# Optimization experiments

Measured on AMD Instinct MI355X. Metric: run time of the kernel, lower is better.

Reference implementation:

```python
import jax, jax.numpy as jnp
import numpy as np

PSIZE = 3
PSTRIDE = 3
N = PSIZE * PSTRIDE   # 9 attention tokens
P = PSIZE ** 2        # 9 pixels per token


def setup_inputs() -> dict:
    key = jax.random.key(0)
    k1, k2, k3, k4, k5 = jax.random.split(key, 5)
    B, H, W, C = 8192, 9, 9, 256
    hidden = C // 2
    x = jax.random.normal(k1, (B, H, W, C), dtype=jnp.float32)
    W_fc = jax.random.normal(k2, (hidden, C), dtype=jnp.float32) * (C ** -0.5)
    b_fc = jax.random.normal(k3, (hidden,), dtype=jnp.float32) * 0.01
    block_idx = jax.random.randint(k4, (B,), 0, 1024, dtype=jnp.int32)
    match_vec = jax.random.randint(k5, (1024, 1), 0, 2, dtype=jnp.int32)
    return {"x": x, "W_fc": W_fc, "b_fc": b_fc, "block_idx": block_idx, "match_vec": match_vec}


def reference(x, W_fc, b_fc, block_idx, match_vec):
    B, H, Wd, C = x.shape
    hidden = W_fc.shape[0]
    scale = (hidden * P) ** -0.5

    # [B, pstride, psize, pstride, psize, C] -> patch-major [B, ps, ps, p, p, C]
    xv = x.reshape(B, PSTRIDE, PSIZE, PSTRIDE, PSIZE, C).transpose(0, 1, 3, 2, 4, 5)
    x_fc = xv.reshape(B, N, P, C)

    # linear projection C -> hidden, then flatten pixels: q [B, N, P*hidden]
    q = (jnp.einsum('bnpc,hc->bnph', x_fc, W_fc) + b_fc).reshape(B, N, P * hidden)

    attn = jnp.einsum('bnd,bmd->bnm', q, q) * scale  # [B, N, N]

    # additive mask: -100 on diagonal, zeroed out entirely for matched samples
    base = jnp.where(jnp.eye(N, dtype=bool), jnp.float32(-100.0), jnp.float32(0.0))
    cur_match = match_vec[block_idx].squeeze(-1)  # [B]
    mask = jnp.where(cur_match[:, None, None] == 1, jnp.float32(0.0), base[None])

    attn = jax.nn.softmax(attn + mask, axis=-1)

    v = xv.reshape(B, N, P * C)
    out = attn @ v  # [B, N, P*C]

    out = out.reshape(B, PSTRIDE, PSTRIDE, PSIZE, PSIZE, C)
    out = out.transpose(0, 1, 3, 2, 4, 5).reshape(B, H, Wd, C)
    return out
```

## Files before the change

### kernel.cpp

```cpp
#include <hip/hip_runtime.h>

typedef short short8 __attribute__((ext_vector_type(8)));
typedef float floatx16 __attribute__((ext_vector_type(16)));
typedef float floatx4 __attribute__((ext_vector_type(4)));
typedef unsigned int uint4v __attribute__((ext_vector_type(4)));

#define ROWS 81
#define CDIM 256
#define QOFF 41472
#define SOFF 62208
#define ABOFF 63232
#define SMEM_TOTAL 63744

__device__ __forceinline__ unsigned short f2bf(float f) {
    union { float f; unsigned int u; } v; v.f = f;
    return (unsigned short)((v.u + 0x7FFFu + ((v.u >> 16) & 1u)) >> 16);
}

__global__ void wconv_kernel(const float* __restrict__ W,
                             unsigned short* __restrict__ Wb, int n) {
    int i = blockIdx.x * 256 + threadIdx.x;
    if (i < n) Wb[i] = f2bf(W[i]);
}

__global__ __launch_bounds__(512, 4)
void attn_kernel(const float* __restrict__ x,
                 const unsigned short* __restrict__ Wb,
                 const float* __restrict__ b_fc,
                 const int* __restrict__ block_idx,
                 const int* __restrict__ match_vec,
                 float* __restrict__ out)
{
    __shared__ __align__(16) char smem[SMEM_TOTAL];
    const int b     = blockIdx.x;
    const int t     = threadIdx.x;
    const int lane  = t & 63;
    const int wave  = t >> 6;
    const int l15   = lane & 15;
    const int kg    = lane >> 4;
    const int l31   = lane & 31;
    const int khalf = lane >> 5;

    int cur_match = 0;
    if (t < 9) cur_match = match_vec[block_idx[b]];

    short8 wfrag[8];
    {
        const unsigned short* wr = Wb + (wave * 16 + l15) * CDIM + kg * 8;
#pragma unroll
        for (int ks = 0; ks < 8; ++ks)
            wfrag[ks] = *(const short8*)(wr + ks * 32);
    }
    const float bias = b_fc[wave * 16 + l15];

    {
        const float* xb = x + (long)b * (ROWS * CDIM);
        for (int k = t; k < ROWS * 32; k += 512) {
            int gr = k >> 5;
            int c0 = (k & 31) * 8;
            float4 a0 = *(const float4*)(xb + gr * CDIM + c0);
            float4 a1 = *(const float4*)(xb + gr * CDIM + c0 + 4);
            int hh = gr / 9, ww = gr % 9;
            int r = ((hh / 3) * 3 + (ww / 3)) * 9 + ((hh % 3) * 3 + (ww % 3));
            short8 v;
            v[0] = (short)f2bf(a0.x); v[1] = (short)f2bf(a0.y);
            v[2] = (short)f2bf(a0.z); v[3] = (short)f2bf(a0.w);
            v[4] = (short)f2bf(a1.x); v[5] = (short)f2bf(a1.y);
            v[6] = (short)f2bf(a1.z); v[7] = (short)f2bf(a1.w);
            int off = r * 512 + ((c0 * 2) ^ ((r & 15) << 4));
            *(short8*)(smem + off) = v;
        }
    }
    __syncthreads();

    floatx4 acc[6];
#pragma unroll
    for (int i = 0; i < 6; ++i)
#pragma unroll
        for (int j = 0; j < 4; ++j) acc[i][j] = 0.f;
    const int swl = l15 << 4;
#pragma unroll
    for (int ks = 0; ks < 8; ++ks) {
        int cb = ks * 64 + kg * 16;
#pragma unroll
        for (int tile = 0; tile < 6; ++tile) {
            int r = tile * 16 + l15;
            short8 a = *(const short8*)(smem + r * 512 + (cb ^ swl));
            acc[tile] = __builtin_amdgcn_mfma_f32_16x16x32_bf16(a, wfrag[ks], acc[tile], 0, 0, 0);
        }
    }

    {
        int h2 = (wave * 16 + l15) * 2;
#pragma unroll
        for (int tile = 0; tile < 6; ++tile) {
#pragma unroll
            for (int reg = 0; reg < 4; ++reg) {
                int r = tile * 16 + kg * 4 + reg;
                if (r < ROWS)
                    *(unsigned short*)(smem + QOFF + r * 256 + (h2 ^ ((r & 15) << 4))) =
                        f2bf(acc[tile][reg] + bias);
            }
        }
    }
    __syncthreads();

    if (wave == 0) {
        floatx4 s0, s1, s2, s3;
#pragma unroll
        for (int i = 0; i < 4; ++i) { s0[i] = 0.f; s1[i] = 0.f; s2[i] = 0.f; s3[i] = 0.f; }
        int nc = (l15 < 9) ? l15 : 8;
#pragma unroll
        for (int s = 0; s < 9; ++s) {
#pragma unroll
            for (int i = 0; i < 4; ++i) {
                int ks = i * 9 + s;
                int k  = ks * 32 + kg * 8;
                int p  = k >> 7;
                int h0 = (k & 127) * 2;
                int row = nc * 9 + p;
                short8 f = *(const short8*)(smem + QOFF + row * 256 + (h0 ^ ((row & 15) << 4)));
                floatx4 tmp = __builtin_amdgcn_mfma_f32_16x16x32_bf16(f, f, (i==0?s0:i==1?s1:i==2?s2:s3), 0, 0, 0);
                if (i == 0) s0 = tmp; else if (i == 1) s1 = tmp; else if (i == 2) s2 = tmp; else s3 = tmp;
            }
        }
        float* sc = (float*)(smem + SOFF);
#pragma unroll
        for (int reg = 0; reg < 4; ++reg)
            sc[(kg * 4 + reg) * 16 + l15] = s0[reg] + s1[reg] + s2[reg] + s3[reg];
    }
    __syncthreads();

    if (t < 9) {
        const float scale = 0.029462782549439483f;
        float* sc = (float*)(smem + SOFF);
        float s[9];
        float mx = -1e30f;
#pragma unroll
        for (int m = 0; m < 9; ++m) {
            float v = sc[t * 16 + m] * scale;
            if (m == t && cur_match != 1) v -= 100.f;
            s[m] = v;
            mx = fmaxf(mx, v);
        }
        float sum = 0.f;
#pragma unroll
        for (int m = 0; m < 9; ++m) { s[m] = __expf(s[m] - mx); sum += s[m]; }
        float inv = 1.f / sum;
        unsigned short* ab = (unsigned short*)(smem + ABOFF) + t * 16;
#pragma unroll
        for (int m = 0; m < 9; ++m) ab[m] = f2bf(s[m] * inv);
#pragma unroll
        for (int m = 9; m < 16; ++m) ab[m] = 0;
    }
    __syncthreads();

    {
        const int n  = l31;
        const int nm = (n < 9) ? n : 0;
        short8 bf = *(const short8*)(smem + ABOFF + nm * 32 + khalf * 16);
        float* ob = out + (long)b * (ROWS * CDIM);
        int hh = 0, ww = 0;
        if (n < 9) { hh = (n / 3) * 3; ww = (n % 3) * 3; }
#pragma unroll
        for (int tt = 0; tt < 9; ++tt) {
            int tile = wave * 9 + tt;
            int d = tile * 32 + l31;
            int p = d >> 8, c = d & 255;
            short8 af;
#pragma unroll
            for (int j = 0; j < 8; ++j) {
                int m = khalf * 8 + j; if (m > 8) m = 8;
                int row = m * 9 + p;
                af[j] = *(const short*)(smem + row * 512 + ((c * 2) ^ ((row & 15) << 4)));
            }
            floatx16 dacc;
#pragma unroll
            for (int i = 0; i < 16; ++i) dacc[i] = 0.f;
            dacc = __builtin_amdgcn_mfma_f32_32x32x16_bf16(af, bf, dacc, 0, 0, 0);
            if (n < 9) {
#pragma unroll
                for (int q2 = 0; q2 < 4; ++q2) {
                    int d0 = tile * 32 + q2 * 8 + khalf * 4;
                    int p0 = d0 >> 8, c0 = d0 & 255;
                    int gr = (hh + (p0 / 3)) * 9 + (ww + (p0 % 3));
                    *(float4*)(ob + gr * CDIM + c0) =
                        make_float4(dacc[q2 * 4 + 0], dacc[q2 * 4 + 1],
                                    dacc[q2 * 4 + 2], dacc[q2 * 4 + 3]);
                }
            }
        }
    }
}

extern "C" void kernel_launch(void* const* d_in, const int* in_sizes, int n_in,
                              void* d_out, int out_size, void* d_ws, size_t ws_size,
                              hipStream_t stream) {
    const float* x    = (const float*)d_in[0];
    const float* W    = (const float*)d_in[1];
    const float* bfc  = (const float*)d_in[2];
    const int*   bidx = (const int*)d_in[3];
    const int*   mvec = (const int*)d_in[4];
    float* outp = (float*)d_out;
    unsigned short* Wb = (unsigned short*)d_ws;

    int nW = in_sizes[1];
    wconv_kernel<<<(nW + 255) / 256, 256, 0, stream>>>(W, Wb, nW);

    int B = in_sizes[0] / (ROWS * CDIM);
    attn_kernel<<<B, 512, 0, stream>>>(x, Wb, bfc, bidx, mvec, outp);
}
```

Before: 371.4 us.

## Make attention kernel persistent with register prefetch of next sample

Launches a fixed grid of 512 blocks, each looping over a contiguous range of batch samples. W fragments and bias are loaded once per block. The next sample's input is prefetched into registers in two halves while the current sample's projection and score phases run, then written to shared memory after the output phase. This hides global load latency and amortizes per-block setup. The cost is higher register pressure, an extra barrier per iteration, and only 512 blocks, which may leave CUs underfilled relative to 4 blocks per CU.

```diff
diff --git a/kernel.cpp b/kernel.cpp
--- a/kernel.cpp
+++ b/kernel.cpp
@@ -3,7 +3,6 @@
 typedef short short8 __attribute__((ext_vector_type(8)));
 typedef float floatx16 __attribute__((ext_vector_type(16)));
 typedef float floatx4 __attribute__((ext_vector_type(4)));
-typedef unsigned int uint4v __attribute__((ext_vector_type(4)));
 
 #define ROWS 81
 #define CDIM 256
@@ -23,16 +22,29 @@
     if (i < n) Wb[i] = f2bf(W[i]);
 }
 
+__device__ __forceinline__ void stage_store(char* smem, int k, float4 a0, float4 a1) {
+    int gr = k >> 5;
+    int c0 = (k & 31) * 8;
+    int hh = gr / 9, ww = gr - hh * 9;
+    int r = ((hh / 3) * 3 + (ww / 3)) * 9 + ((hh % 3) * 3 + (ww % 3));
+    short8 v;
+    v[0] = (short)f2bf(a0.x); v[1] = (short)f2bf(a0.y);
+    v[2] = (short)f2bf(a0.z); v[3] = (short)f2bf(a0.w);
+    v[4] = (short)f2bf(a1.x); v[5] = (short)f2bf(a1.y);
+    v[6] = (short)f2bf(a1.z); v[7] = (short)f2bf(a1.w);
+    *(short8*)(smem + r * 512 + ((c0 * 2) ^ ((r & 15) << 4))) = v;
+}
+
 __global__ __launch_bounds__(512, 4)
 void attn_kernel(const float* __restrict__ x,
                  const unsigned short* __restrict__ Wb,
                  const float* __restrict__ b_fc,
                  const int* __restrict__ block_idx,
                  const int* __restrict__ match_vec,
-                 float* __restrict__ out)
+                 float* __restrict__ out,
+                 int B, int nIter)
 {
     __shared__ __align__(16) char smem[SMEM_TOTAL];
-    const int b     = blockIdx.x;
     const int t     = threadIdx.x;
     const int lane  = t & 63;
     const int wave  = t >> 6;
@@ -40,9 +52,8 @@
     const int kg    = lane >> 4;
     const int l31   = lane & 31;
     const int khalf = lane >> 5;
-
-    int cur_match = 0;
-    if (t < 9) cur_match = match_vec[block_idx[b]];
+    const int base  = blockIdx.x * nIter;
+    if (base >= B) return;
 
     short8 wfrag[8];
     {
@@ -52,144 +63,193 @@
             wfrag[ks] = *(const short8*)(wr + ks * 32);
     }
     const float bias = b_fc[wave * 16 + l15];
+    const int swl = l15 << 4;
 
     {
-        const float* xb = x + (long)b * (ROWS * CDIM);
-        for (int k = t; k < ROWS * 32; k += 512) {
-            int gr = k >> 5;
-            int c0 = (k & 31) * 8;
-            float4 a0 = *(const float4*)(xb + gr * CDIM + c0);
-            float4 a1 = *(const float4*)(xb + gr * CDIM + c0 + 4);
-            int hh = gr / 9, ww = gr % 9;
-            int r = ((hh / 3) * 3 + (ww / 3)) * 9 + ((hh % 3) * 3 + (ww % 3));
-            short8 v;
-            v[0] = (short)f2bf(a0.x); v[1] = (short)f2bf(a0.y);
-            v[2] = (short)f2bf(a0.z); v[3] = (short)f2bf(a0.w);
-            v[4] = (short)f2bf(a1.x); v[5] = (short)f2bf(a1.y);
-            v[6] = (short)f2bf(a1.z); v[7] = (short)f2bf(a1.w);
-            int off = r * 512 + ((c0 * 2) ^ ((r & 15) << 4));
-            *(short8*)(smem + off) = v;
-        }
+        const float* xb = x + (size_t)base * (ROWS * CDIM);
+        float4 a0[3], a1[3];
+#pragma unroll
+        for (int j = 0; j < 3; ++j) {
+            int k = t + 512 * j;
+            a0[j] = *(const float4*)(xb + k * 8);
+            a1[j] = *(const float4*)(xb + k * 8 + 4);
+        }
+#pragma unroll
+        for (int j = 0; j < 3; ++j) stage_store(smem, t + 512 * j, a0[j], a1[j]);
+#pragma unroll
+        for (int j = 0; j < 2; ++j) {
+            int k = t + 1536 + 512 * j;
+            a0[j] = *(const float4*)(xb + k * 8);
+            a1[j] = *(const float4*)(xb + k * 8 + 4);
+        }
+        if (t < 32) {
+            a0[2] = *(const float4*)(xb + (t + 2560) * 8);
+            a1[2] = *(const float4*)(xb + (t + 2560) * 8 + 4);
+        }
+#pragma unroll
+        for (int j = 0; j < 2; ++j) stage_store(smem, t + 1536 + 512 * j, a0[j], a1[j]);
+        if (t < 32) stage_store(smem, t + 2560, a0[2], a1[2]);
     }
     __syncthreads();
 
-    floatx4 acc[6];
-#pragma unroll
-    for (int i = 0; i < 6; ++i)
-#pragma unroll
-        for (int j = 0; j < 4; ++j) acc[i][j] = 0.f;
-    const int swl = l15 << 4;
-#pragma unroll
-    for (int ks = 0; ks < 8; ++ks) {
-        int cb = ks * 64 + kg * 16;
-#pragma unroll
-        for (int tile = 0; tile < 6; ++tile) {
-            int r = tile * 16 + l15;
-            short8 a = *(const short8*)(smem + r * 512 + (cb ^ swl));
-            acc[tile] = __builtin_amdgcn_mfma_f32_16x16x32_bf16(a, wfrag[ks], acc[tile], 0, 0, 0);
-        }
-    }
-
-    {
-        int h2 = (wave * 16 + l15) * 2;
-#pragma unroll
-        for (int tile = 0; tile < 6; ++tile) {
-#pragma unroll
-            for (int reg = 0; reg < 4; ++reg) {
-                int r = tile * 16 + kg * 4 + reg;
-                if (r < ROWS)
-                    *(unsigned short*)(smem + QOFF + r * 256 + (h2 ^ ((r & 15) << 4))) =
-                        f2bf(acc[tile][reg] + bias);
-            }
-        }
-    }
-    __syncthreads();
-
-    if (wave == 0) {
-        floatx4 s0, s1, s2, s3;
-#pragma unroll
-        for (int i = 0; i < 4; ++i) { s0[i] = 0.f; s1[i] = 0.f; s2[i] = 0.f; s3[i] = 0.f; }
-        int nc = (l15 < 9) ? l15 : 8;
-#pragma unroll
-        for (int s = 0; s < 9; ++s) {
-#pragma unroll
-            for (int i = 0; i < 4; ++i) {
-                int ks = i * 9 + s;
-                int k  = ks * 32 + kg * 8;
-                int p  = k >> 7;
-                int h0 = (k & 127) * 2;
-                int row = nc * 9 + p;
-                short8 f = *(const short8*)(smem + QOFF + row * 256 + (h0 ^ ((row & 15) << 4)));
-                floatx4 tmp = __builtin_amdgcn_mfma_f32_16x16x32_bf16(f, f, (i==0?s0:i==1?s1:i==2?s2:s3), 0, 0, 0);
-                if (i == 0) s0 = tmp; else if (i == 1) s1 = tmp; else if (i == 2) s2 = tmp; else s3 = tmp;
-            }
-        }
-        float* sc = (float*)(smem + SOFF);
-#pragma unroll
-        for (int reg = 0; reg < 4; ++reg)
-            sc[(kg * 4 + reg) * 16 + l15] = s0[reg] + s1[reg] + s2[reg] + s3[reg];
-    }
-    __syncthreads();
-
-    if (t < 9) {
-        const float scale = 0.029462782549439483f;
-        float* sc = (float*)(smem + SOFF);
-        float s[9];
-        float mx = -1e30f;
-#pragma unroll
-        for (int m = 0; m < 9; ++m) {
-            float v = sc[t * 16 + m] * scale;
-            if (m == t && cur_match != 1) v -= 100.f;
-            s[m] = v;
-            mx = fmaxf(mx, v);
-        }
-        float sum = 0.f;
-#pragma unroll
-        for (int m = 0; m < 9; ++m) { s[m] = __expf(s[m] - mx); sum += s[m]; }
-        float inv = 1.f / sum;
-        unsigned short* ab = (unsigned short*)(smem + ABOFF) + t * 16;
-#pragma unroll
-        for (int m = 0; m < 9; ++m) ab[m] = f2bf(s[m] * inv);
-#pragma unroll
-        for (int m = 9; m < 16; ++m) ab[m] = 0;
-    }
-    __syncthreads();
-
-    {
-        const int n  = l31;
-        const int nm = (n < 9) ? n : 0;
-        short8 bf = *(const short8*)(smem + ABOFF + nm * 32 + khalf * 16);
-        float* ob = out + (long)b * (ROWS * CDIM);
-        int hh = 0, ww = 0;
-        if (n < 9) { hh = (n / 3) * 3; ww = (n % 3) * 3; }
-#pragma unroll
-        for (int tt = 0; tt < 9; ++tt) {
-            int tile = wave * 9 + tt;
-            int d = tile * 32 + l31;
-            int p = d >> 8, c = d & 255;
-            short8 af;
-#pragma unroll
-            for (int j = 0; j < 8; ++j) {
-                int m = khalf * 8 + j; if (m > 8) m = 8;
-                int row = m * 9 + p;
-                af[j] = *(const short*)(smem + row * 512 + ((c * 2) ^ ((row & 15) << 4)));
-            }
-            floatx16 dacc;
-#pragma unroll
-            for (int i = 0; i < 16; ++i) dacc[i] = 0.f;
-            dacc = __builtin_amdgcn_mfma_f32_32x32x16_bf16(af, bf, dacc, 0, 0, 0);
-            if (n < 9) {
-#pragma unroll
-                for (int q2 = 0; q2 < 4; ++q2) {
-                    int d0 = tile * 32 + q2 * 8 + khalf * 4;
-                    int p0 = d0 >> 8, c0 = d0 & 255;
-                    int gr = (hh + (p0 / 3)) * 9 + (ww + (p0 % 3));
-                    *(float4*)(ob + gr * CDIM + c0) =
-                        make_float4(dacc[q2 * 4 + 0], dacc[q2 * 4 + 1],
-                                    dacc[q2 * 4 + 2], dacc[q2 * 4 + 3]);
-                }
-            }
-        }
+    for (int i = 0; base + i < B && i < nIter; ++i) {
+        const int b = base + i;
+        const bool hasNext = (i + 1 < nIter) && (b + 1 < B);
+        const float* xn = x + (size_t)(b + 1) * (ROWS * CDIM);
+
+        float4 n10[3], n11[3];
+        if (hasNext) {
+#pragma unroll
+            for (int j = 0; j < 3; ++j) {
+                int k = t + 512 * j;
+                n10[j] = *(const float4*)(xn + k * 8);
+                n11[j] = *(const float4*)(xn + k * 8 + 4);
+            }
+        }
+        int cm = 0;
+        if (t < 9) cm = match_vec[block_idx[b]];
+
+        {
+            floatx4 acc[6];
+#pragma unroll
+            for (int ii = 0; ii < 6; ++ii)
+#pragma unroll
+                for (int j = 0; j < 4; ++j) acc[ii][j] = 0.f;
+#pragma unroll
+            for (int ks = 0; ks < 8; ++ks) {
+                int cb = ks * 64 + kg * 16;
+#pragma unroll
+                for (int tile = 0; tile < 6; ++tile) {
+                    int r = tile * 16 + l15;
+                    short8 a = *(const short8*)(smem + r * 512 + (cb ^ swl));
+                    acc[tile] = __builtin_amdgcn_mfma_f32_16x16x32_bf16(a, wfrag[ks], acc[tile], 0, 0, 0);
+                }
+            }
+            int h2 = (wave * 16 + l15) * 2;
+#pragma unroll
+            for (int tile = 0; tile < 6; ++tile) {
+#pragma unroll
+                for (int reg = 0; reg < 4; ++reg) {
+                    int r = tile * 16 + kg * 4 + reg;
+                    if (r < ROWS)
+                        *(unsigned short*)(smem + QOFF + r * 256 + (h2 ^ ((r & 15) << 4))) =
+                            f2bf(acc[tile][reg] + bias);
+                }
+            }
+        }
+        __syncthreads();
+
+        float4 n20[2], n21[2], n30, n31;
+        if (hasNext) {
+#pragma unroll
+            for (int j = 0; j < 2; ++j) {
+                int k = t + 1536 + 512 * j;
+                n20[j] = *(const float4*)(xn + k * 8);
+                n21[j] = *(const float4*)(xn + k * 8 + 4);
+            }
+            if (t < 32) {
+                n30 = *(const float4*)(xn + (t + 2560) * 8);
+                n31 = *(const float4*)(xn + (t + 2560) * 8 + 4);
+            }
+        }
+
+        if (wave == 0) {
+            floatx4 s0, s1, s2, s3;
+#pragma unroll
+            for (int ii = 0; ii < 4; ++ii) { s0[ii] = 0.f; s1[ii] = 0.f; s2[ii] = 0.f; s3[ii] = 0.f; }
+            int nc = (l15 < 9) ? l15 : 8;
+#pragma unroll
+            for (int s = 0; s < 9; ++s) {
+#pragma unroll
+                for (int ii = 0; ii < 4; ++ii) {
+                    int ks = ii * 9 + s;
+                    int k  = ks * 32 + kg * 8;
+                    int p  = k >> 7;
+                    int h0 = (k & 127) * 2;
+                    int row = nc * 9 + p;
+                    short8 f = *(const short8*)(smem + QOFF + row * 256 + (h0 ^ ((row & 15) << 4)));
+                    floatx4 tmp = __builtin_amdgcn_mfma_f32_16x16x32_bf16(
+                        f, f, (ii == 0 ? s0 : ii == 1 ? s1 : ii == 2 ? s2 : s3), 0, 0, 0);
+                    if (ii == 0) s0 = tmp; else if (ii == 1) s1 = tmp; else if (ii == 2) s2 = tmp; else s3 = tmp;
+                }
+            }
+            float* sc = (float*)(smem + SOFF);
+#pragma unroll
+            for (int reg = 0; reg < 4; ++reg)
+                sc[(kg * 4 + reg) * 16 + l15] = s0[reg] + s1[reg] + s2[reg] + s3[reg];
+        }
+        __syncthreads();
+
+        if (t < 9) {
+            const float scale = 0.029462782549439483f;
+            float* sc = (float*)(smem + SOFF);
+            float s[9];
+            float mx = -1e30f;
+#pragma unroll
+            for (int m = 0; m < 9; ++m) {
+                float v = sc[t * 16 + m] * scale;
+                if (m == t && cm != 1) v -= 100.f;
+                s[m] = v;
+                mx = fmaxf(mx, v);
+            }
+            float sum = 0.f;
+#pragma unroll
+            for (int m = 0; m < 9; ++m) { s[m] = __expf(s[m] - mx); sum += s[m]; }
+            float inv = 1.f / sum;
+            unsigned short* ab = (unsigned short*)(smem + ABOFF) + t * 16;
+#pragma unroll
+            for (int m = 0; m < 9; ++m) ab[m] = f2bf(s[m] * inv);
+#pragma unroll
+            for (int m = 9; m < 16; ++m) ab[m] = 0;
+        }
+        __syncthreads();
+
+        {
+            const int n  = l31;
+            const int nm = (n < 9) ? n : 0;
+            short8 bf = *(const short8*)(smem + ABOFF + nm * 32 + khalf * 16);
+            float* ob = out + (size_t)b * (ROWS * CDIM);
+            int hh = 0, ww = 0;
+            if (n < 9) { hh = (n / 3) * 3; ww = (n % 3) * 3; }
+#pragma unroll
+            for (int tt = 0; tt < 9; ++tt) {
+                int tile = wave * 9 + tt;
+                int d = tile * 32 + l31;
+                int p = d >> 8, c = d & 255;
+                short8 af;
+#pragma unroll
+                for (int j = 0; j < 8; ++j) {
+                    int m = khalf * 8 + j; if (m > 8) m = 8;
+                    int row = m * 9 + p;
+                    af[j] = *(const short*)(smem + row * 512 + ((c * 2) ^ ((row & 15) << 4)));
+                }
+                floatx16 dacc;
+#pragma unroll
+                for (int ii = 0; ii < 16; ++ii) dacc[ii] = 0.f;
+                dacc = __builtin_amdgcn_mfma_f32_32x32x16_bf16(af, bf, dacc, 0, 0, 0);
+                if (n < 9) {
+#pragma unroll
+                    for (int q2 = 0; q2 < 4; ++q2) {
+                        int d0 = tile * 32 + q2 * 8 + khalf * 4;
+                        int p0 = d0 >> 8, c0 = d0 & 255;
+                        int gr = (hh + (p0 / 3)) * 9 + (ww + (p0 % 3));
+                        *(float4*)(ob + gr * CDIM + c0) =
+                            make_float4(dacc[q2 * 4 + 0], dacc[q2 * 4 + 1],
+                                        dacc[q2 * 4 + 2], dacc[q2 * 4 + 3]);
+                    }
+                }
+            }
+        }
+        __syncthreads();
+
+        if (hasNext) {
+#pragma unroll
+            for (int j = 0; j < 3; ++j) stage_store(smem, t + 512 * j, n10[j], n11[j]);
+#pragma unroll
+            for (int j = 0; j < 2; ++j) stage_store(smem, t + 1536 + 512 * j, n20[j], n21[j]);
+            if (t < 32) stage_store(smem, t + 2560, n30, n31);
+        }
+        __syncthreads();
     }
 }
 
@@ -208,5 +268,7 @@
     wconv_kernel<<<(nW + 255) / 256, 256, 0, stream>>>(W, Wb, nW);
 
     int B = in_sizes[0] / (ROWS * CDIM);
-    attn_kernel<<<B, 512, 0, stream>>>(x, Wb, bfc, bidx, mvec, outp);
-}
+    int grid = (B >= 512) ? 512 : B;
+    int nIter = (B + grid - 1) / grid;
+    attn_kernel<<<grid, 512, 0, stream>>>(x, Wb, bfc, bidx, mvec, outp, B, nIter);
+}
```

Measured after the change: 978.6 us. +163.5%, slower.

## Halve Q staging buffer and split Gram computation across all waves

Applied to the files above, without the earlier changes.

The projected Q matrix is now staged in LDS in two 64-column halves instead of one full buffer, which cuts shared memory from about 63.7KB to 53.4KB. The launch-bounds occupancy hint rises from 4 to 6 blocks. The Gram (QQ^T) computation is spread across all 8 waves, which accumulate partial scores with LDS atomicAdd, replacing the single wave 0 that did it before. The cost is two extra barriers, atomic contention on the score buffer, and a changed token-major row layout for x in LDS.

```diff
diff --git a/kernel.cpp b/kernel.cpp
--- a/kernel.cpp
+++ b/kernel.cpp
@@ -3,14 +3,14 @@
 typedef short short8 __attribute__((ext_vector_type(8)));
 typedef float floatx16 __attribute__((ext_vector_type(16)));
 typedef float floatx4 __attribute__((ext_vector_type(4)));
-typedef unsigned int uint4v __attribute__((ext_vector_type(4)));
 
 #define ROWS 81
 #define CDIM 256
-#define QOFF 41472
-#define SOFF 62208
-#define ABOFF 63232
-#define SMEM_TOTAL 63744
+#define XT   0
+#define QH   41472
+#define SC   51840
+#define AB   52864
+#define TOT  53376
 
 __device__ __forceinline__ unsigned short f2bf(float f) {
     union { float f; unsigned int u; } v; v.f = f;
@@ -23,7 +23,7 @@
     if (i < n) Wb[i] = f2bf(W[i]);
 }
 
-__global__ __launch_bounds__(512, 4)
+__global__ __launch_bounds__(512, 6)
 void attn_kernel(const float* __restrict__ x,
                  const unsigned short* __restrict__ Wb,
                  const float* __restrict__ b_fc,
@@ -31,7 +31,7 @@
                  const int* __restrict__ match_vec,
                  float* __restrict__ out)
 {
-    __shared__ __align__(16) char smem[SMEM_TOTAL];
+    __shared__ __align__(16) char smem[TOT];
     const int b     = blockIdx.x;
     const int t     = threadIdx.x;
     const int lane  = t & 63;
@@ -41,8 +41,8 @@
     const int l31   = lane & 31;
     const int khalf = lane >> 5;
 
-    int cur_match = 0;
-    if (t < 9) cur_match = match_vec[block_idx[b]];
+    int cm = 0;
+    if (t < 9) cm = match_vec[block_idx[b]];
 
     short8 wfrag[8];
     {
@@ -53,22 +53,25 @@
     }
     const float bias = b_fc[wave * 16 + l15];
 
+    if (t < 256) ((float*)(smem + SC))[t] = 0.f;
+
     {
-        const float* xb = x + (long)b * (ROWS * CDIM);
+        const float* xb = x + (size_t)b * (ROWS * CDIM);
         for (int k = t; k < ROWS * 32; k += 512) {
             int gr = k >> 5;
             int c0 = (k & 31) * 8;
             float4 a0 = *(const float4*)(xb + gr * CDIM + c0);
             float4 a1 = *(const float4*)(xb + gr * CDIM + c0 + 4);
-            int hh = gr / 9, ww = gr % 9;
-            int r = ((hh / 3) * 3 + (ww / 3)) * 9 + ((hh % 3) * 3 + (ww % 3));
+            int hh = gr / 9, ww = gr - hh * 9;
+            int p = (hh % 3) * 3 + (ww % 3);
+            int m = (hh / 3) * 3 + (ww / 3);
+            int r = p * 9 + m;
             short8 v;
             v[0] = (short)f2bf(a0.x); v[1] = (short)f2bf(a0.y);
             v[2] = (short)f2bf(a0.z); v[3] = (short)f2bf(a0.w);
             v[4] = (short)f2bf(a1.x); v[5] = (short)f2bf(a1.y);
             v[6] = (short)f2bf(a1.z); v[7] = (short)f2bf(a1.w);
-            int off = r * 512 + ((c0 * 2) ^ ((r & 15) << 4));
-            *(short8*)(smem + off) = v;
+            *(short8*)(smem + XT + r * 512 + ((c0 * 2) ^ ((r & 15) << 4))) = v;
         }
     }
     __syncthreads();
@@ -85,61 +88,70 @@
 #pragma unroll
         for (int tile = 0; tile < 6; ++tile) {
             int r = tile * 16 + l15;
-            short8 a = *(const short8*)(smem + r * 512 + (cb ^ swl));
+            short8 a = *(const short8*)(smem + XT + r * 512 + (cb ^ swl));
             acc[tile] = __builtin_amdgcn_mfma_f32_16x16x32_bf16(a, wfrag[ks], acc[tile], 0, 0, 0);
         }
     }
 
-    {
+    if (wave < 4) {
         int h2 = (wave * 16 + l15) * 2;
 #pragma unroll
-        for (int tile = 0; tile < 6; ++tile) {
+        for (int tile = 0; tile < 6; ++tile)
 #pragma unroll
             for (int reg = 0; reg < 4; ++reg) {
                 int r = tile * 16 + kg * 4 + reg;
                 if (r < ROWS)
-                    *(unsigned short*)(smem + QOFF + r * 256 + (h2 ^ ((r & 15) << 4))) =
+                    *(unsigned short*)(smem + QH + r * 128 + (h2 ^ ((r & 7) << 4))) =
                         f2bf(acc[tile][reg] + bias);
             }
-        }
-    }
-    __syncthreads();
-
-    if (wave == 0) {
-        floatx4 s0, s1, s2, s3;
-#pragma unroll
-        for (int i = 0; i < 4; ++i) { s0[i] = 0.f; s1[i] = 0.f; s2[i] = 0.f; s3[i] = 0.f; }
-        int nc = (l15 < 9) ? l15 : 8;
-#pragma unroll
-        for (int s = 0; s < 9; ++s) {
-#pragma unroll
-            for (int i = 0; i < 4; ++i) {
-                int ks = i * 9 + s;
-                int k  = ks * 32 + kg * 8;
-                int p  = k >> 7;
-                int h0 = (k & 127) * 2;
-                int row = nc * 9 + p;
-                short8 f = *(const short8*)(smem + QOFF + row * 256 + (h0 ^ ((row & 15) << 4)));
-                floatx4 tmp = __builtin_amdgcn_mfma_f32_16x16x32_bf16(f, f, (i==0?s0:i==1?s1:i==2?s2:s3), 0, 0, 0);
-                if (i == 0) s0 = tmp; else if (i == 1) s1 = tmp; else if (i == 2) s2 = tmp; else s3 = tmp;
-            }
-        }
-        float* sc = (float*)(smem + SOFF);
-#pragma unroll
-        for (int reg = 0; reg < 4; ++reg)
-            sc[(kg * 4 + reg) * 16 + l15] = s0[reg] + s1[reg] + s2[reg] + s3[reg];
-    }
+    }
+    __syncthreads();
+
+    const int nc = (l15 < 9) ? l15 : 8;
+#define GRAM_HALF()                                                                 \
+    {                                                                               \
+        floatx4 g; g[0] = 0.f; g[1] = 0.f; g[2] = 0.f; g[3] = 0.f;                  \
+        for (int ks = wave; ks < 18; ks += 8) {                                     \
+            int p  = ks >> 1;                                                       \
+            int h0 = (ks & 1) * 64 + kg * 16;           \
+            int row = p * 9 + nc;                                                   \
+            short8 f = *(const short8*)(smem + QH + row * 128 +                     \
+                                        (h0 ^ ((row & 7) << 4)));                   \
+            g = __builtin_amdgcn_mfma_f32_16x16x32_bf16(f, f, g, 0, 0, 0);          \
+        }                                                                           \
+        float* sc = (float*)(smem + SC);                                            \
+        _Pragma("unroll")                                                           \
+        for (int reg = 0; reg < 4; ++reg)                                           \
+            atomicAdd(&sc[(kg * 4 + reg) * 16 + l15], g[reg]);                      \
+    }
+    GRAM_HALF();
+    __syncthreads();
+
+    if (wave >= 4) {
+        int h2 = ((wave - 4) * 16 + l15) * 2;
+#pragma unroll
+        for (int tile = 0; tile < 6; ++tile)
+#pragma unroll
+            for (int reg = 0; reg < 4; ++reg) {
+                int r = tile * 16 + kg * 4 + reg;
+                if (r < ROWS)
+                    *(unsigned short*)(smem + QH + r * 128 + (h2 ^ ((r & 7) << 4))) =
+                        f2bf(acc[tile][reg] + bias);
+            }
+    }
+    __syncthreads();
+    GRAM_HALF();
     __syncthreads();
 
     if (t < 9) {
         const float scale = 0.029462782549439483f;
-        float* sc = (float*)(smem + SOFF);
+        float* sc = (float*)(smem + SC);
         float s[9];
         float mx = -1e30f;
 #pragma unroll
         for (int m = 0; m < 9; ++m) {
             float v = sc[t * 16 + m] * scale;
-            if (m == t && cur_match != 1) v -= 100.f;
+            if (m == t && cm != 1) v -= 100.f;
             s[m] = v;
             mx = fmaxf(mx, v);
         }
@@ -147,7 +159,7 @@
 #pragma unroll
         for (int m = 0; m < 9; ++m) { s[m] = __expf(s[m] - mx); sum += s[m]; }
         float inv = 1.f / sum;
-        unsigned short* ab = (unsigned short*)(smem + ABOFF) + t * 16;
+        unsigned short* ab = (unsigned short*)(smem + AB) + t * 16;
 #pragma unroll
         for (int m = 0; m < 9; ++m) ab[m] = f2bf(s[m] * inv);
 #pragma unroll
@@ -158,10 +170,10 @@
     {
         const int n  = l31;
         const int nm = (n < 9) ? n : 0;
-        short8 bf = *(const short8*)(smem + ABOFF + nm * 32 + khalf * 16);
-        float* ob = out + (long)b * (ROWS * CDIM);
-        int hh = 0, ww = 0;
-        if (n < 9) { hh = (n / 3) * 3; ww = (n % 3) * 3; }
+        short8 bf = *(const short8*)(smem + AB + nm * 32 + khalf * 16);
+        float* ob = out + (size_t)b * (ROWS * CDIM);
+        int hh0 = 0, ww0 = 0;
+        if (n < 9) { hh0 = (n / 3) * 3; ww0 = (n % 3) * 3; }
 #pragma unroll
         for (int tt = 0; tt < 9; ++tt) {
             int tile = wave * 9 + tt;
@@ -170,9 +182,9 @@
             short8 af;
 #pragma unroll
             for (int j = 0; j < 8; ++j) {
-                int m = khalf * 8 + j; if (m > 8) m = 8;
-                int row = m * 9 + p;
-                af[j] = *(const short*)(smem + row * 512 + ((c * 2) ^ ((row & 15) << 4)));
+                int mm = khalf * 8 + j; if (mm > 8) mm = 8;
+                int row = p * 9 + mm;
+                af[j] = *(const short*)(smem + XT + row * 512 + ((c * 2) ^ ((row & 15) << 4)));
             }
             floatx16 dacc;
 #pragma unroll
@@ -183,7 +195,7 @@
                 for (int q2 = 0; q2 < 4; ++q2) {
                     int d0 = tile * 32 + q2 * 8 + khalf * 4;
                     int p0 = d0 >> 8, c0 = d0 & 255;
-                    int gr = (hh + (p0 / 3)) * 9 + (ww + (p0 % 3));
+                    int gr = (hh0 + p0 / 3) * 9 + (ww0 + p0 % 3);
                     *(float4*)(ob + gr * CDIM + c0) =
                         make_float4(dacc[q2 * 4 + 0], dacc[q2 * 4 + 1],
                                     dacc[q2 * 4 + 2], dacc[q2 * 4 + 3]);
```

Result: slower. 417.3 us (+12.3%).

## Make attention kernel persistent with async LDS prefetch of next sample

Applied to the files above, without the earlier changes.

Replaces one-block-per-sample with 256 persistent 1024-thread blocks that each loop over many samples. The next sample's fp32 input is fetched straight into LDS with global_load_lds while the current sample is converted and computed, to overlap memory latency with compute. Work is split across 16 waves. The large LDS footprint limits residency to one block per CU, and the per-sample barrier chain is serialised.

```diff
diff --git a/kernel.cpp b/kernel.cpp
--- a/kernel.cpp
+++ b/kernel.cpp
@@ -1,16 +1,22 @@
 #include <hip/hip_runtime.h>
 
 typedef short short8 __attribute__((ext_vector_type(8)));
+typedef short short4v __attribute__((ext_vector_type(4)));
 typedef float floatx16 __attribute__((ext_vector_type(16)));
 typedef float floatx4 __attribute__((ext_vector_type(4)));
-typedef unsigned int uint4v __attribute__((ext_vector_type(4)));
 
 #define ROWS 81
 #define CDIM 256
-#define QOFF 41472
-#define SOFF 62208
-#define ABOFF 63232
-#define SMEM_TOTAL 63744
+#define XT   0
+#define RAW  41472
+#define QOFF 124416
+#define SC   145152
+#define AB   146176
+#define TOT  146688
+
+typedef const __attribute__((address_space(1))) unsigned int* gas_ptr;
+typedef __attribute__((address_space(3))) unsigned int* las_ptr;
+#define GLOAD16(g, l) __builtin_amdgcn_global_load_lds((gas_ptr)(g), (las_ptr)(l), 16, 0, 0)
 
 __device__ __forceinline__ unsigned short f2bf(float f) {
     union { float f; unsigned int u; } v; v.f = f;
@@ -23,16 +29,16 @@
     if (i < n) Wb[i] = f2bf(W[i]);
 }
 
-__global__ __launch_bounds__(512, 4)
+__global__ __launch_bounds__(1024, 4)
 void attn_kernel(const float* __restrict__ x,
                  const unsigned short* __restrict__ Wb,
                  const float* __restrict__ b_fc,
                  const int* __restrict__ block_idx,
                  const int* __restrict__ match_vec,
-                 float* __restrict__ out)
+                 float* __restrict__ out,
+                 int B, int nIter)
 {
-    __shared__ __align__(16) char smem[SMEM_TOTAL];
-    const int b     = blockIdx.x;
+    __shared__ __align__(16) char smem[TOT];
     const int t     = threadIdx.x;
     const int lane  = t & 63;
     const int wave  = t >> 6;
@@ -40,156 +46,166 @@
     const int kg    = lane >> 4;
     const int l31   = lane & 31;
     const int khalf = lane >> 5;
-
-    int cur_match = 0;
-    if (t < 9) cur_match = match_vec[block_idx[b]];
+    const int hgrp  = wave & 7;
+    const int rhalf = wave >> 3;
+    const int base  = blockIdx.x * nIter;
+    if (base >= B) return;
 
     short8 wfrag[8];
     {
-        const unsigned short* wr = Wb + (wave * 16 + l15) * CDIM + kg * 8;
+        const unsigned short* wr = Wb + (hgrp * 16 + l15) * CDIM + kg * 8;
 #pragma unroll
         for (int ks = 0; ks < 8; ++ks)
             wfrag[ks] = *(const short8*)(wr + ks * 32);
     }
-    const float bias = b_fc[wave * 16 + l15];
+    const float bias = b_fc[hgrp * 16 + l15];
+    const int swl = l15 << 4;
 
     {
-        const float* xb = x + (long)b * (ROWS * CDIM);
-        for (int k = t; k < ROWS * 32; k += 512) {
-            int gr = k >> 5;
-            int c0 = (k & 31) * 8;
-            float4 a0 = *(const float4*)(xb + gr * CDIM + c0);
-            float4 a1 = *(const float4*)(xb + gr * CDIM + c0 + 4);
-            int hh = gr / 9, ww = gr % 9;
-            int r = ((hh / 3) * 3 + (ww / 3)) * 9 + ((hh % 3) * 3 + (ww % 3));
-            short8 v;
-            v[0] = (short)f2bf(a0.x); v[1] = (short)f2bf(a0.y);
-            v[2] = (short)f2bf(a0.z); v[3] = (short)f2bf(a0.w);
-            v[4] = (short)f2bf(a1.x); v[5] = (short)f2bf(a1.y);
-            v[6] = (short)f2bf(a1.z); v[7] = (short)f2bf(a1.w);
-            int off = r * 512 + ((c0 * 2) ^ ((r & 15) << 4));
-            *(short8*)(smem + off) = v;
-        }
+        const float* xb = x + (size_t)base * (ROWS * CDIM);
+        for (int u = t; u < 5184; u += 1024)
+            GLOAD16(xb + u * 4, smem + RAW + u * 16);
     }
     __syncthreads();
 
-    floatx4 acc[6];
-#pragma unroll
-    for (int i = 0; i < 6; ++i)
-#pragma unroll
-        for (int j = 0; j < 4; ++j) acc[i][j] = 0.f;
-    const int swl = l15 << 4;
-#pragma unroll
-    for (int ks = 0; ks < 8; ++ks) {
-        int cb = ks * 64 + kg * 16;
-#pragma unroll
-        for (int tile = 0; tile < 6; ++tile) {
-            int r = tile * 16 + l15;
-            short8 a = *(const short8*)(smem + r * 512 + (cb ^ swl));
-            acc[tile] = __builtin_amdgcn_mfma_f32_16x16x32_bf16(a, wfrag[ks], acc[tile], 0, 0, 0);
-        }
-    }
-
-    {
-        int h2 = (wave * 16 + l15) * 2;
-#pragma unroll
-        for (int tile = 0; tile < 6; ++tile) {
-#pragma unroll
-            for (int reg = 0; reg < 4; ++reg) {
-                int r = tile * 16 + kg * 4 + reg;
-                if (r < ROWS)
-                    *(unsigned short*)(smem + QOFF + r * 256 + (h2 ^ ((r & 15) << 4))) =
-                        f2bf(acc[tile][reg] + bias);
-            }
-        }
-    }
-    __syncthreads();
-
-    if (wave == 0) {
-        floatx4 s0, s1, s2, s3;
-#pragma unroll
-        for (int i = 0; i < 4; ++i) { s0[i] = 0.f; s1[i] = 0.f; s2[i] = 0.f; s3[i] = 0.f; }
-        int nc = (l15 < 9) ? l15 : 8;
-#pragma unroll
-        for (int s = 0; s < 9; ++s) {
-#pragma unroll
-            for (int i = 0; i < 4; ++i) {
-                int ks = i * 9 + s;
-                int k  = ks * 32 + kg * 8;
-                int p  = k >> 7;
-                int h0 = (k & 127) * 2;
-                int row = nc * 9 + p;
-                short8 f = *(const short8*)(smem + QOFF + row * 256 + (h0 ^ ((row & 15) << 4)));
-                floatx4 tmp = __builtin_amdgcn_mfma_f32_16x16x32_bf16(f, f, (i==0?s0:i==1?s1:i==2?s2:s3), 0, 0, 0);
-                if (i == 0) s0 = tmp; else if (i == 1) s1 = tmp; else if (i == 2) s2 = tmp; else s3 = tmp;
-            }
-        }
-        float* sc = (float*)(smem + SOFF);
-#pragma unroll
-        for (int reg = 0; reg < 4; ++reg)
-            sc[(kg * 4 + reg) * 16 + l15] = s0[reg] + s1[reg] + s2[reg] + s3[reg];
-    }
-    __syncthreads();
-
-    if (t < 9) {
-        const float scale = 0.029462782549439483f;
-        float* sc = (float*)(smem + SOFF);
-        float s[9];
-        float mx = -1e30f;
-#pragma unroll
-        for (int m = 0; m < 9; ++m) {
-            float v = sc[t * 16 + m] * scale;
-            if (m == t && cur_match != 1) v -= 100.f;
-            s[m] = v;
-            mx = fmaxf(mx, v);
-        }
-        float sum = 0.f;
-#pragma unroll
-        for (int m = 0; m < 9; ++m) { s[m] = __expf(s[m] - mx); sum += s[m]; }
-        float inv = 1.f / sum;
-        unsigned short* ab = (unsigned short*)(smem + ABOFF) + t * 16;
-#pragma unroll
-        for (int m = 0; m < 9; ++m) ab[m] = f2bf(s[m] * inv);
-#pragma unroll
-        for (int m = 9; m < 16; ++m) ab[m] = 0;
-    }
-    __syncthreads();
-
-    {
-        const int n  = l31;
-        const int nm = (n < 9) ? n : 0;
-        short8 bf = *(const short8*)(smem + ABOFF + nm * 32 + khalf * 16);
-        float* ob = out + (long)b * (ROWS * CDIM);
-        int hh = 0, ww = 0;
-        if (n < 9) { hh = (n / 3) * 3; ww = (n % 3) * 3; }
-#pragma unroll
-        for (int tt = 0; tt < 9; ++tt) {
-            int tile = wave * 9 + tt;
-            int d = tile * 32 + l31;
-            int p = d >> 8, c = d & 255;
-            short8 af;
-#pragma unroll
-            for (int j = 0; j < 8; ++j) {
-                int m = khalf * 8 + j; if (m > 8) m = 8;
-                int row = m * 9 + p;
-                af[j] = *(const short*)(smem + row * 512 + ((c * 2) ^ ((row & 15) << 4)));
-            }
-            floatx16 dacc;
-#pragma unroll
-            for (int i = 0; i < 16; ++i) dacc[i] = 0.f;
-            dacc = __builtin_amdgcn_mfma_f32_32x32x16_bf16(af, bf, dacc, 0, 0, 0);
-            if (n < 9) {
-#pragma unroll
-                for (int q2 = 0; q2 < 4; ++q2) {
-                    int d0 = tile * 32 + q2 * 8 + khalf * 4;
-                    int p0 = d0 >> 8, c0 = d0 & 255;
-                    int gr = (hh + (p0 / 3)) * 9 + (ww + (p0 % 3));
-                    *(float4*)(ob + gr * CDIM + c0) =
-                        make_float4(dacc[q2 * 4 + 0], dacc[q2 * 4 + 1],
-                                    dacc[q2 * 4 + 2], dacc[q2 * 4 + 3]);
-                }
-            }
-        }
+    for (int it = 0; it < nIter; ++it) {
+        const int b = base + it;
+        if (b >= B) break;
+        int cm = 0;
+        if (t < 9) cm = match_vec[block_idx[b]];
+
+        for (int u = t; u < 5184; u += 1024) {
+            float4 a = *(const float4*)(smem + RAW + u * 16);
+            int gr = u >> 6;
+            int c0 = (u & 63) * 4;
+            int hh = gr / 9, ww = gr - hh * 9;
+            int r = ((hh / 3) * 3 + ww / 3) * 9 + (hh % 3) * 3 + (ww % 3);
+            short4v v;
+            v[0] = (short)f2bf(a.x); v[1] = (short)f2bf(a.y);
+            v[2] = (short)f2bf(a.z); v[3] = (short)f2bf(a.w);
+            *(short4v*)(smem + XT + r * 512 + ((c0 * 2) ^ ((r & 15) << 4))) = v;
+        }
+        __syncthreads();
+
+        if (it + 1 < nIter && b + 1 < B) {
+            const float* xn = x + (size_t)(b + 1) * (ROWS * CDIM);
+            for (int u = t; u < 5184; u += 1024)
+                GLOAD16(xn + u * 4, smem + RAW + u * 16);
+        }
+
+        {
+            floatx4 acc[3];
+#pragma unroll
+            for (int i = 0; i < 3; ++i)
+#pragma unroll
+                for (int j = 0; j < 4; ++j) acc[i][j] = 0.f;
+#pragma unroll
+            for (int ks = 0; ks < 8; ++ks) {
+                int cb = ks * 64 + kg * 16;
+#pragma unroll
+                for (int tile = 0; tile < 3; ++tile) {
+                    int r = rhalf * 48 + tile * 16 + l15;
+                    short8 a = *(const short8*)(smem + XT + r * 512 + (cb ^ swl));
+                    acc[tile] = __builtin_amdgcn_mfma_f32_16x16x32_bf16(a, wfrag[ks], acc[tile], 0, 0, 0);
+                }
+            }
+            int h2 = (hgrp * 16 + l15) * 2;
+#pragma unroll
+            for (int tile = 0; tile < 3; ++tile)
+#pragma unroll
+                for (int reg = 0; reg < 4; ++reg) {
+                    int r = rhalf * 48 + tile * 16 + kg * 4 + reg;
+                    if (r < ROWS)
+                        *(unsigned short*)(smem + QOFF + r * 256 + (h2 ^ ((r & 15) << 4))) =
+                            f2bf(acc[tile][reg] + bias);
+                }
+        }
+        __syncthreads();
+
+        if (wave == 0) {
+            floatx4 s0, s1, s2, s3;
+#pragma unroll
+            for (int ii = 0; ii < 4; ++ii) { s0[ii] = 0.f; s1[ii] = 0.f; s2[ii] = 0.f; s3[ii] = 0.f; }
+            int nc = (l15 < 9) ? l15 : 8;
+#pragma unroll
+            for (int s = 0; s < 9; ++s) {
+#pragma unroll
+                for (int ii = 0; ii < 4; ++ii) {
+                    int ks = ii * 9 + s;
+                    int k  = ks * 32 + kg * 8;
+                    int p  = k >> 7;
+                    int h0 = (k & 127) * 2;
+                    int row = nc * 9 + p;
+                    short8 f = *(const short8*)(smem + QOFF + row * 256 + (h0 ^ ((row & 15) << 4)));
+                    floatx4 tmp = __builtin_amdgcn_mfma_f32_16x16x32_bf16(
+                        f, f, (ii == 0 ? s0 : ii == 1 ? s1 : ii == 2 ? s2 : s3), 0, 0, 0);
+                    if (ii == 0) s0 = tmp; else if (ii == 1) s1 = tmp; else if (ii == 2) s2 = tmp; else s3 = tmp;
+                }
+            }
+            float* sc = (float*)(smem + SC);
+#pragma unroll
+            for (int reg = 0; reg < 4; ++reg)
+                sc[(kg * 4 + reg) * 16 + l15] = s0[reg] + s1[reg] + s2[reg] + s3[reg];
+
+            if (lane < 9) {
+                const float scale = 0.029462782549439483f;
+                float s[9];
+                float mx = -1e30f;
+#pragma unroll
+                for (int m = 0; m < 9; ++m) {
+                    float v = sc[lane * 16 + m] * scale;
+                    if (m == lane && cm != 1) v -= 100.f;
+                    s[m] = v;
+                    mx = fmaxf(mx, v);
+                }
+                float sum = 0.f;
+#pragma unroll
+                for (int m = 0; m < 9; ++m) { s[m] = __expf(s[m] - mx); sum += s[m]; }
+                float inv = 1.f / sum;
+                unsigned short* ab = (unsigned short*)(smem + AB) + lane * 16;
+#pragma unroll
+                for (int m = 0; m < 9; ++m) ab[m] = f2bf(s[m] * inv);
+#pragma unroll
+                for (int m = 9; m < 16; ++m) ab[m] = 0;
+            }
+        }
+        __syncthreads();
+
+        {
+            const int n  = l31;
+            const int nm = (n < 9) ? n : 0;
+            short8 bf = *(const short8*)(smem + AB + nm * 32 + khalf * 16);
+            float* ob = out + (size_t)b * (ROWS * CDIM);
+            int hh0 = 0, ww0 = 0;
+            if (n < 9) { hh0 = (n / 3) * 3; ww0 = (n % 3) * 3; }
+            for (int tile = wave; tile < 72; tile += 16) {
+                int d = tile * 32 + l31;
+                int p = d >> 8, c = d & 255;
+                short8 af;
+#pragma unroll
+                for (int j = 0; j < 8; ++j) {
+                    int mm = khalf * 8 + j; if (mm > 8) mm = 8;
+                    int row = mm * 9 + p;
+                    af[j] = *(const short*)(smem + XT + row * 512 + ((c * 2) ^ ((row & 15) << 4)));
+                }
+                floatx16 dacc;
+#pragma unroll
+                for (int ii = 0; ii < 16; ++ii) dacc[ii] = 0.f;
+                dacc = __builtin_amdgcn_mfma_f32_32x32x16_bf16(af, bf, dacc, 0, 0, 0);
+                if (n < 9) {
+#pragma unroll
+                    for (int q2 = 0; q2 < 4; ++q2) {
+                        int d0 = tile * 32 + q2 * 8 + khalf * 4;
+                        int p0 = d0 >> 8, c0 = d0 & 255;
+                        int gr = (hh0 + p0 / 3) * 9 + (ww0 + p0 % 3);
+                        *(float4*)(ob + gr * CDIM + c0) =
+                            make_float4(dacc[q2 * 4 + 0], dacc[q2 * 4 + 1],
+                                        dacc[q2 * 4 + 2], dacc[q2 * 4 + 3]);
+                    }
+                }
+            }
+        }
+        __syncthreads();
     }
 }
 
@@ -208,5 +224,7 @@
     wconv_kernel<<<(nW + 255) / 256, 256, 0, stream>>>(W, Wb, nW);
 
     int B = in_sizes[0] / (ROWS * CDIM);
-    attn_kernel<<<B, 512, 0, stream>>>(x, Wb, bfc, bidx, mvec, outp);
-}
+    int grid = (B < 256) ? B : 256;
+    int nIter = (B + grid - 1) / grid;
+    attn_kernel<<<grid, 1024, 0, stream>>>(x, Wb, bfc, bidx, mvec, outp, B, nIter);
+}
```

Result: slower. 531.6 us (+43.1%).
